# Optimization experiments

Hardware: AMD Instinct MI355X
Metric: run time of the kernel (lower is better)

The kernel has to match this reference:

```python
import jax, jax.numpy as jnp
import numpy as np

NUM_CLASSES = 19
IGNORE = 255
KLD_MARGIN = 3.0
DEC = 0.01
BOT_EPS, TOP_EPS = 1e-4, 1.0
# eight-corner neighbor offsets (size=1), order matches AAF layers.eightcorner_activation
EDGE_OFFS = ((-1, -1), (-1, 0), (-1, 1), (0, -1), (0, 1), (1, -1), (1, 0), (1, 1))


def _shift(x, dy, dx, pad_val):
    # Shift along H,W (axes 1,2): out[:, y, x] = x[:, y+dy, x+dx], padded with pad_val.
    pads = [(0, 0), (1, 1), (1, 1)] + [(0, 0)] * (x.ndim - 3)
    xp = jnp.pad(x, pads, constant_values=pad_val)
    h, w = x.shape[1], x.shape[2]
    return xp[:, 1 + dy:1 + dy + h, 1 + dx:1 + dx + w]


def _resize_bilinear_ac(x, oh, ow):
    # torch F.interpolate(mode='bilinear', align_corners=True) on NCHW.
    n, c, h, w = x.shape
    ys = jnp.linspace(0.0, h - 1.0, oh)
    xs = jnp.linspace(0.0, w - 1.0, ow)
    y0 = jnp.floor(ys).astype(jnp.int32); y1 = jnp.minimum(y0 + 1, h - 1)
    x0 = jnp.floor(xs).astype(jnp.int32); x1 = jnp.minimum(x0 + 1, w - 1)
    wy = (ys - y0).astype(x.dtype)[None, None, :, None]
    wx = (xs - x0).astype(x.dtype)[None, None, None, :]
    rows = x[:, :, y0, :] * (1.0 - wy) + x[:, :, y1, :] * wy  # (N,C,oh,W)
    return rows[:, :, :, x0] * (1.0 - wx) + rows[:, :, :, x1] * wx  # (N,C,oh,ow)


def setup_inputs() -> dict:
    key = jax.random.key(0)
    k1, k2 = jax.random.split(key)
    preds = jax.random.normal(k1, (2, NUM_CLASSES, 64, 64), dtype=jnp.float32)
    targets = jax.random.randint(k2, (2, 512, 512), 0, NUM_CLASSES, dtype=jnp.int32)
    w_edge = jnp.zeros((1, 1, 1, NUM_CLASSES, 1, 3), dtype=jnp.float32)
    w_not_edge = jnp.zeros((1, 1, 1, NUM_CLASSES, 1, 3), dtype=jnp.float32)
    return {"preds": preds, "targets": targets, "w_edge": w_edge, "w_not_edge": w_not_edge}


def reference(preds, targets, w_edge, w_not_edge):
    h, w = targets.shape[1], targets.shape[2]
    pred = _resize_bilinear_ac(preds, h, w)          # (N,C,H,W)
    prob = jax.nn.softmax(pred, axis=1)
    prob = jnp.transpose(prob, (0, 2, 3, 1))          # (N,H,W,C) NHWC layout used by AAF layers

    labels = targets                                  # (N,H,W)
    ign = labels == IGNORE
    one_label = jnp.where(ign, 0, labels)
    ohl = jax.nn.one_hot(one_label, NUM_CLASSES, dtype=jnp.float32)  # (N,H,W,C)
    ohl = jnp.where(ign[..., None], float(IGNORE), ohl)

    # edge/non-edge class weights: softmax over last dim, take index 0 -> (1,1,1,C,1)
    w_e = jax.nn.softmax(w_edge, axis=-1)[..., 0]
    w_ne = jax.nn.softmax(w_not_edge, axis=-1)[..., 0]

    # ignores_from_label: bidirectional ignore mask, neighbor order is reversed offsets
    ignore_c = labels > NUM_CLASSES - 1               # (N,H,W)
    ignore8 = jnp.stack([_shift(ignore_c, -dy, -dx, True) | ignore_c for dy, dx in EDGE_OFFS], axis=-1)
    not_ignore = ~ignore8[:, :, :, None, :]           # (N,H,W,1,8)

    # edges_from_label: neighbor label (padded with ignore_class) differs from center
    edge8 = jnp.stack([_shift(ohl, dy, dx, float(IGNORE)) != ohl for dy, dx in EDGE_OFFS], axis=-1)  # (N,H,W,C,8)
    edge = edge8 & not_ignore
    not_edge = (~edge) & not_ignore

    # eightcorner_activation on probabilities (zero padded)
    probs_paired = jnp.stack([_shift(prob, dy, dx, 0.0) for dy, dx in EDGE_OFFS], axis=-1)  # (N,H,W,C,8)
    p = prob[..., None]                               # (N,H,W,C,1)
    pc = jnp.clip(p, BOT_EPS, TOP_EPS)
    npc = jnp.clip(1.0 - p, BOT_EPS, TOP_EPS)
    ppc = jnp.clip(probs_paired, BOT_EPS, TOP_EPS)
    nppc = jnp.clip(1.0 - probs_paired, BOT_EPS, TOP_EPS)

    # binary KL divergence per class/neighbor
    kldiv = ppc * jnp.log(ppc / pc) + nppc * jnp.log(nppc / npc)  # (N,H,W,C,8)

    # per-pixel class weights: sum_c w[c]*one_hot[c] -> (N,H,W,1,1)
    we_map = jnp.sum(w_e * ohl[..., None], axis=3, keepdims=True)
    wne_map = jnp.sum(w_ne * ohl[..., None], axis=3, keepdims=True)

    edge_loss = jnp.maximum(0.0, KLD_MARGIN - kldiv) * we_map
    not_edge_loss = kldiv * wne_map

    # torch.mean over gathered nonzero indices == masked sum / count
    e_cnt = jnp.maximum(jnp.sum(edge), 1).astype(jnp.float32)
    ne_cnt = jnp.maximum(jnp.sum(not_edge), 1).astype(jnp.float32)
    e_mean = jnp.sum(jnp.where(edge, edge_loss, 0.0)) / e_cnt
    ne_mean = jnp.sum(jnp.where(not_edge, not_edge_loss, 0.0)) / ne_cnt

    return e_mean * 1.0 * DEC + ne_mean * 1.0 * DEC
```

## Files before the change

### kernel.cpp

```cpp
#include <hip/hip_runtime.h>
#include <stdint.h>


#define NC 19
#define HH 512
#define WW 512
#define NB 2
#define TS 16
#define HS 18
#define HP (HS * HS)
#define ATRS 20
#define PS 25
#define NBLK 2048
#define LOG2E 1.4426950408889634f
#define LN2 0.6931471805599453f
#define LOG2EPS -13.287712379549449f
#define K2F 4.3280851226668906f
#define K2PAD 4.328125f

typedef _Float16 f16x2 __attribute__((ext_vector_type(2)));

#if __has_builtin(__builtin_amdgcn_exp2f)
#define EXP2F(x) __builtin_amdgcn_exp2f(x)
#else
#define EXP2F(x) __expf((x) * LN2)
#endif

#if __has_builtin(__builtin_amdgcn_fdot2)
#define FDOT2(a, b, c) __builtin_amdgcn_fdot2((a), (b), (c), false)
#else
#define FDOT2(a, b, c) fmaf((float)(a)[1], (float)(b)[1], fmaf((float)(a)[0], (float)(b)[0], (c)))
#endif

struct Part { float es, ns; unsigned int cnt, pad; };

union U32F2 { uint32_t u; f16x2 h; };
__device__ __forceinline__ uint32_t bc_u32(f16x2 v) { U32F2 x; x.h = v; return x.u; }
__device__ __forceinline__ f16x2 bc_h2(uint32_t v) { U32F2 x; x.u = v; return x.h; }
__device__ __forceinline__ float extf(f16x2 v, int h) { return h ? (float)v[1] : (float)v[0]; }

union U16H { uint16_t u; _Float16 h; };
__device__ __forceinline__ uint32_t pack_TL(int lab, float T) {
    U16H t; t.h = (_Float16)T;
    return ((uint32_t)lab << 16) | (uint32_t)t.u;
}
__device__ __forceinline__ float TL_T(uint32_t tl) {
    U16H t; t.u = (uint16_t)(tl & 0xFFFFu);
    return (float)t.h;
}

template <bool KEEP>
__device__ __forceinline__ int pix_compute(const float* __restrict__ patch,
                                           const int* __restrict__ tg,
                                           int y, int x, int y0b, int x0b,
                                           uint32_t* __restrict__ ATrow,
                                           uint32_t* __restrict__ TLw,
                                           f16x2* __restrict__ Dh,
                                           float* __restrict__ SLp) {
    const bool oob = ((unsigned)y >= (unsigned)HH) | ((unsigned)x >= (unsigned)WW);
    if (oob) {
        const _Float16 aP = (_Float16)1e-4f;
        const uint32_t aPP = bc_u32((f16x2){aP, aP});
        const uint32_t aPL = bc_u32((f16x2){aP, (_Float16)0.0f});
        uint2 wv;
        wv.x = aPP; wv.y = aPP;
        *reinterpret_cast<uint2*>(ATrow + 0) = wv;
        *reinterpret_cast<uint2*>(ATrow + 2) = wv;
        *reinterpret_cast<uint2*>(ATrow + 4) = wv;
        *reinterpret_cast<uint2*>(ATrow + 6) = wv;
        wv.y = aPL;
        *reinterpret_cast<uint2*>(ATrow + 8) = wv;
        uint2 zv; zv.x = 0u; zv.y = 0u;
        *reinterpret_cast<uint2*>(ATrow + 10) = zv;
        *reinterpret_cast<uint2*>(ATrow + 12) = zv;
        *reinterpret_cast<uint2*>(ATrow + 14) = zv;
        *reinterpret_cast<uint2*>(ATrow + 16) = zv;
        *reinterpret_cast<uint2*>(ATrow + 18) = zv;
        *TLw = pack_TL(255, 0.0f);
        if (KEEP) {
            const _Float16 dP = (_Float16)LOG2EPS;
#pragma unroll
            for (int j = 0; j < 10; ++j)
                Dh[j] = (j < 9) ? (f16x2){dP, dP} : (f16x2){dP, (_Float16)0.0f};
            *SLp = 0.0f;
        }
        return 255;
    }

    const int lab = tg[(y << 9) + x];
    const float fy = (float)(y * 63) / 511.0f;
    const float fx = (float)(x * 63) / 511.0f;
    const int y0 = (int)fy, x0 = (int)fx;
    const float wy = fy - (float)y0, wx = fx - (float)x0;
    const int y1 = min(y0 + 1, 63), x1 = min(x0 + 1, 63);
    const float omwy = 1.0f - wy, omwx = 1.0f - wx;
    const float bw00 = omwy * omwx, bw01 = omwy * wx;
    const float bw10 = wy * omwx,   bw11 = wy * wx;
    const int o00 = (y0 - y0b) * 5 + (x0 - x0b);
    const int o01 = o00 + (x1 - x0);
    const int o10 = o00 + (y1 - y0) * 5;
    const int o11 = o10 + (x1 - x0);

    float v2[NC];
    float s = 0.0f;
#pragma unroll
    for (int c = 0; c < NC; ++c) {
        const float* pc_ = &patch[c * PS];
        const float vv = fmaf(pc_[o00], bw00, fmaf(pc_[o01], bw01,
                          fmaf(pc_[o10], bw10, pc_[o11] * bw11)));
        v2[c] = vv;
        s += EXP2F(vv);
    }
    const float lns2 = __log2f(s);

    float Tdd = 0.0f, SL = 0.0f;
#pragma unroll
    for (int jp = 0; jp < 10; jp += 2) {
        uint32_t aw0 = 0u, aw1 = 0u, lw0 = 0u, lw1 = 0u;
#pragma unroll
        for (int q = 0; q < 2; ++q) {
            const int j = jp + q;
            _Float16 a0h = (_Float16)0.0f, l0h = (_Float16)0.0f, d0h = (_Float16)0.0f;
            _Float16 a1h = (_Float16)0.0f, l1h = (_Float16)0.0f, d1h = (_Float16)0.0f;
            {
                const int c = 2 * j;
                const float lr = v2[c] - lns2;
                const float p = EXP2F(lr);
                const float la = fmaxf(lr, LOG2EPS);
                const float aa = fmaxf(p, 1e-4f);
                const float lb = __log2f(fmaxf(1.0f - p, 1e-4f));
                const float dd = la - lb;
                Tdd = fmaf(aa, dd, Tdd); SL += lb;
                a0h = (_Float16)aa; l0h = (_Float16)lb; d0h = (_Float16)dd;
            }
            if (2 * j + 1 < NC) {
                const int c = 2 * j + 1;
                const float lr = v2[c] - lns2;
                const float p = EXP2F(lr);
                const float la = fmaxf(lr, LOG2EPS);
                const float aa = fmaxf(p, 1e-4f);
                const float lb = __log2f(fmaxf(1.0f - p, 1e-4f));
                const float dd = la - lb;
                Tdd = fmaf(aa, dd, Tdd); SL += lb;
                a1h = (_Float16)aa; l1h = (_Float16)lb; d1h = (_Float16)dd;
            }
            if (q == 0) { aw0 = bc_u32((f16x2){a0h, a1h}); lw0 = bc_u32((f16x2){l0h, l1h}); }
            else        { aw1 = bc_u32((f16x2){a0h, a1h}); lw1 = bc_u32((f16x2){l0h, l1h}); }
            if (KEEP) Dh[j] = (f16x2){d0h, d1h};
        }
        uint2 av; av.x = aw0; av.y = aw1;
        uint2 lv; lv.x = lw0; lv.y = lw1;
        *reinterpret_cast<uint2*>(ATrow + jp) = av;
        *reinterpret_cast<uint2*>(ATrow + 10 + jp) = lv;
    }
    *TLw = pack_TL(lab, Tdd + SL);
    if (KEEP) *SLp = SL;
    return lab;
}

__global__ __launch_bounds__(256, 5) void k_fused(const float* __restrict__ preds,
                                                  const int* __restrict__ targets,
                                                  const float* __restrict__ w_edge,
                                                  const float* __restrict__ w_not_edge,
                                                  Part* __restrict__ pb) {
    __shared__ __align__(16) uint32_t AT[HP * ATRS];
    __shared__ uint32_t TL[HP];
    __shared__ float2 swen[NC];
    __shared__ float patch[NC * PS];
    __shared__ float r_es[4], r_ns[4];
    __shared__ unsigned int r_cnt[4];

    const int tid = threadIdx.x;
    const int bx = blockIdx.x, by = blockIdx.y, n = blockIdx.z;

    if (tid < NC) {
        float sw_e, sw_n;
        {
            float a = w_edge[tid * 3 + 0], b = w_edge[tid * 3 + 1], c = w_edge[tid * 3 + 2];
            float m = fmaxf(a, fmaxf(b, c));
            float ea = __expf(a - m), eb = __expf(b - m), ec = __expf(c - m);
            sw_e = (ea / (ea + eb + ec)) * LN2;
        }
        {
            float a = w_not_edge[tid * 3 + 0], b = w_not_edge[tid * 3 + 1], c = w_not_edge[tid * 3 + 2];
            float m = fmaxf(a, fmaxf(b, c));
            float ea = __expf(a - m), eb = __expf(b - m), ec = __expf(c - m);
            sw_n = (ea / (ea + eb + ec)) * LN2;
        }
        swen[tid] = make_float2(sw_e, sw_n);
    }

    const int* tg = targets + (n << 18);
    const float* pbase = preds + (size_t)n * NC * 4096;

    const int ty = tid >> 4, tx = tid & 15;
    const int hi = (ty + 1) * HS + (tx + 1);
    const int DOFF[8] = {-HS - 1, -HS, -HS + 1, -1, 1, HS - 1, HS, HS + 1};
    const int DY[8] = {-1, -1, -1, 0, 0, 1, 1, 1};
    const int DX[8] = {-1, 0, 1, -1, 1, -1, 0, 1};
    const f16x2 one2 = {(_Float16)1.0f, (_Float16)1.0f};
    const f16x2 k32 = {(_Float16)K2F, (_Float16)K2F};

    float e_s = 0.0f, ne_s = 0.0f;
    unsigned int cnt = 0;

    const int yT = max(by * TS - 1, 0), xL = max(bx * TS - 1, 0);
    const int y0b = (yT * 63) / 511, x0b = (xL * 63) / 511;
    for (int t = tid; t < NC * PS; t += 256) {
        const int c = t / PS, r = t - c * PS;
        const int ry = r / 5, rx = r - ry * 5;
        const int sy = min(y0b + ry, 63), sx = min(x0b + rx, 63);
        patch[t] = pbase[c * 4096 + (sy << 6) + sx] * LOG2E;
    }
    __syncthreads();

    if (tid < 68) {
        int i;
        if (tid < 18)      i = tid;
        else if (tid < 36) i = 306 + (tid - 18);
        else if (tid < 52) i = (tid - 35) * HS;
        else               i = (tid - 51) * HS + 17;
        const int hy = i / HS, hx = i - hy * HS;
        pix_compute<false>(patch, tg, by * TS + hy - 1, bx * TS + hx - 1,
                           y0b, x0b, &AT[i * ATRS], &TL[i], nullptr, nullptr);
    }

    const uint32_t* myrow = &AT[hi * ATRS];
    f16x2 Dh[10];
    float SL;
    const int lab = pix_compute<true>(patch, tg, by * TS + ty, bx * TS + tx,
                                      y0b, x0b, &AT[hi * ATRS], &TL[hi], Dh, &SL);
    const int plab = lab >> 1, hlab = lab & 1;
    const float aown = extf(bc_h2(myrow[plab]), hlab);
    const float llab = extf(bc_h2(myrow[10 + plab]), hlab);
    const float dlab = __log2f(aown) - llab;
    const float u = fmaf(aown, dlab, llab);
    __syncthreads();

    const bool interior_blk = (bx > 0) & (bx < 31) & (by > 0) & (by < 31);
    const bool deep_blk = (bx > 1) & (bx < 30) & (by > 1) & (by < 30);
    float es_o = 0.0f, ns_o = 0.0f;
    float es_w = 0.0f, ns_w = 0.0f;

    if (deep_blk) {
#pragma unroll
        for (int k = 0; k < 8; ++k) {
            const int np = hi + DOFF[k];
            const uint32_t tl = TL[np];
            const int nlab = (int)(tl >> 16);
            const float T_N = TL_T(tl);
            const uint32_t* rb = &AT[np * ATRS];
            const uint4 A0 = *reinterpret_cast<const uint4*>(rb);
            const uint4 A1 = *reinterpret_cast<const uint4*>(rb + 4);
            const uint2 A2 = *reinterpret_cast<const uint2*>(rb + 8);
            float acc = 0.0f;
            acc = FDOT2(bc_h2(A0.x), Dh[0], acc);
            acc = FDOT2(bc_h2(A0.y), Dh[1], acc);
            acc = FDOT2(bc_h2(A0.z), Dh[2], acc);
            acc = FDOT2(bc_h2(A0.w), Dh[3], acc);
            acc = FDOT2(bc_h2(A1.x), Dh[4], acc);
            acc = FDOT2(bc_h2(A1.y), Dh[5], acc);
            acc = FDOT2(bc_h2(A1.z), Dh[6], acc);
            acc = FDOT2(bc_h2(A1.w), Dh[7], acc);
            acc = FDOT2(bc_h2(A2.x), Dh[8], acc);
            acc = FDOT2(bc_h2(A2.y), Dh[9], acc);
            const float dot = T_N - acc - SL;
            const float aN = extf(bc_h2(rb[plab]), hlab);
            const float lN = extf(bc_h2(rb[10 + plab]), hlab);
            const float dN = __log2f(aN) - lN;
            const float klL = fmaf(aN, dN, lN) - fmaf(aN, dlab, llab);
            const float klR = u - fmaf(aown, dN, lN);
            const bool df = (lab != nlab);
            const float wg = df ? 1.0f : 0.0f;
            const float2 sw = swen[nlab];
            es_o = fmaf(wg, fmaxf(K2F - klL, 0.0f), es_o);
            ns_o += dot - wg * klL;
            es_w = fmaf(wg * sw.x, fmaxf(K2F - klR, 0.0f), es_w);
            ns_w = fmaf(-wg * sw.y, klR, ns_w);
            cnt += df ? ((2u << 16) | (NC - 2)) : NC;
        }
    } else if (interior_blk) {
        const int gy = by * TS + ty, gx = bx * TS + tx;
#pragma unroll
        for (int k = 0; k < 8; ++k) {
            const int np = hi + DOFF[k];
            const uint32_t tl = TL[np];
            const int nlab = (int)(tl >> 16);
            const float T_N = TL_T(tl);
            const uint32_t* rb = &AT[np * ATRS];
            const uint4 A0 = *reinterpret_cast<const uint4*>(rb);
            const uint4 A1 = *reinterpret_cast<const uint4*>(rb + 4);
            const uint2 A2 = *reinterpret_cast<const uint2*>(rb + 8);
            float acc = 0.0f;
            acc = FDOT2(bc_h2(A0.x), Dh[0], acc);
            acc = FDOT2(bc_h2(A0.y), Dh[1], acc);
            acc = FDOT2(bc_h2(A0.z), Dh[2], acc);
            acc = FDOT2(bc_h2(A0.w), Dh[3], acc);
            acc = FDOT2(bc_h2(A1.x), Dh[4], acc);
            acc = FDOT2(bc_h2(A1.y), Dh[5], acc);
            acc = FDOT2(bc_h2(A1.z), Dh[6], acc);
            acc = FDOT2(bc_h2(A1.w), Dh[7], acc);
            acc = FDOT2(bc_h2(A2.x), Dh[8], acc);
            acc = FDOT2(bc_h2(A2.y), Dh[9], acc);
            const float dot = T_N - acc - SL;
            const float aN = extf(bc_h2(rb[plab]), hlab);
            const float lN = extf(bc_h2(rb[10 + plab]), hlab);
            const float dN = __log2f(aN) - lN;
            const float klL = fmaf(aN, dN, lN) - fmaf(aN, dlab, llab);
            const bool df = (lab != nlab);
            const float wg = df ? 1.0f : 0.0f;
            const int gyN = gy + DY[k], gxN = gx + DX[k];
            const bool E = ((unsigned)(gyN - 16) < 480u) & ((unsigned)(gxN - 16) < 480u);
            if (E) {
                const float klR = u - fmaf(aown, dN, lN);
                const float2 sw = swen[nlab];
                es_o = fmaf(wg, fmaxf(K2F - klL, 0.0f), es_o);
                ns_o += dot - wg * klL;
                es_w = fmaf(wg * sw.x, fmaxf(K2F - klR, 0.0f), es_w);
                ns_w = fmaf(-wg * sw.y, klR, ns_w);
            } else {
                const int pn = nlab >> 1, hn = nlab & 1;
                const float aN2 = extf(bc_h2(rb[pn]), hn);
                const float lN2 = extf(bc_h2(rb[10 + pn]), hn);
                const float dN2 = __log2f(aN2) - lN2;
                const float ao = extf(bc_h2(myrow[pn]), hn);
                const float lo = extf(bc_h2(myrow[10 + pn]), hn);
                const float doo = __log2f(ao) - lo;
                const float klN = fmaf(aN2, dN2, lN2) - fmaf(aN2, doo, lo);
                es_o = fmaf(wg, fmaxf(K2F - klL, 0.0f) + fmaxf(K2F - klN, 0.0f), es_o);
                ns_o += dot - wg * (klL + klN);
            }
            cnt += df ? ((2u << 16) | (NC - 2)) : NC;
        }
    } else if (lab <= NC - 1) {
        const _Float16 aP = (_Float16)1e-4f, dP = (_Float16)LOG2EPS;
        const _Float16 tP = (_Float16)((float)aP * (float)dP);
#pragma unroll
        for (int k = 0; k < 8; ++k) {
            const int off = DOFF[k];
            const int rlab = (int)(TL[hi - off] >> 16);
            const bool rvalid = (rlab <= NC - 1);
            const int np = hi + off;
            const uint32_t tl = TL[np];
            const int nlab = (int)(tl >> 16);
            const bool isPad = (nlab == 255);
            float ek_k, nk_k;
            unsigned int pc;
            if (isPad) {
                float ekall = 0.0f;
#pragma unroll
                for (int j = 0; j < 10; j += 2) {
                    const uint2 lr = *reinterpret_cast<const uint2*>(myrow + 10 + j);
                    const f16x2 l20 = bc_h2(lr.x);
                    const f16x2 l21 = bc_h2(lr.y);
                    const f16x2 a20 = {aP, aP};
                    const f16x2 t20 = {tP, tP};
                    const f16x2 a21 = (j + 1 < 9) ? (f16x2){aP, aP} : (f16x2){aP, (_Float16)0.0f};
                    const f16x2 t21 = (j + 1 < 9) ? (f16x2){tP, tP} : (f16x2){tP, (_Float16)0.0f};
                    f16x2 kl0 = t20 - (a20 * Dh[j] + l20);
                    f16x2 kl1 = t21 - (a21 * Dh[j + 1] + l21);
                    f16x2 m0 = k32 - kl0, m1 = k32 - kl1;
                    m0[0] = m0[0] > (_Float16)0.0f ? m0[0] : (_Float16)0.0f;
                    m0[1] = m0[1] > (_Float16)0.0f ? m0[1] : (_Float16)0.0f;
                    m1[0] = m1[0] > (_Float16)0.0f ? m1[0] : (_Float16)0.0f;
                    m1[1] = m1[1] > (_Float16)0.0f ? m1[1] : (_Float16)0.0f;
                    ekall = FDOT2(m0, one2, ekall);
                    ekall = FDOT2(m1, one2, ekall);
                }
                ek_k = ekall - K2PAD;
                nk_k = 0.0f;
                pc = NC;
            } else {
                const float T_N = TL_T(tl);
                const uint32_t* rb = &AT[np * ATRS];
                const uint4 A0 = *reinterpret_cast<const uint4*>(rb);
                const uint4 A1 = *reinterpret_cast<const uint4*>(rb + 4);
                const uint2 A2 = *reinterpret_cast<const uint2*>(rb + 8);
                float acc = 0.0f;
                acc = FDOT2(bc_h2(A0.x), Dh[0], acc);
                acc = FDOT2(bc_h2(A0.y), Dh[1], acc);
                acc = FDOT2(bc_h2(A0.z), Dh[2], acc);
                acc = FDOT2(bc_h2(A0.w), Dh[3], acc);
                acc = FDOT2(bc_h2(A1.x), Dh[4], acc);
                acc = FDOT2(bc_h2(A1.y), Dh[5], acc);
                acc = FDOT2(bc_h2(A1.z), Dh[6], acc);
                acc = FDOT2(bc_h2(A1.w), Dh[7], acc);
                acc = FDOT2(bc_h2(A2.x), Dh[8], acc);
                acc = FDOT2(bc_h2(A2.y), Dh[9], acc);
                const float dot = T_N - acc - SL;
                const float aN = extf(bc_h2(rb[plab]), hlab);
                const float lN = extf(bc_h2(rb[10 + plab]), hlab);
                const float dN = __log2f(aN) - lN;
                const float klL = fmaf(aN, dN, lN) - fmaf(aN, dlab, llab);
                const int pn = nlab >> 1, hn = nlab & 1;
                const float aN2 = extf(bc_h2(rb[pn]), hn);
                const float lN2 = extf(bc_h2(rb[10 + pn]), hn);
                const float dN2 = __log2f(aN2) - lN2;
                const float ao = extf(bc_h2(myrow[pn]), hn);
                const float lo = extf(bc_h2(myrow[10 + pn]), hn);
                const float doo = __log2f(ao) - lo;
                const float klN = fmaf(aN2, dN2, lN2) - fmaf(aN2, doo, lo);
                const bool df = (lab != nlab);
                const float wg = df ? 1.0f : 0.0f;
                ek_k = wg * (fmaxf(K2F - klL, 0.0f) + fmaxf(K2F - klN, 0.0f));
                nk_k = dot - wg * (klL + klN);
                pc = df ? 2u : 0u;
            }
            const float vf = rvalid ? 1.0f : 0.0f;
            es_o = fmaf(vf, ek_k, es_o);
            ns_o = fmaf(vf, nk_k, ns_o);
            cnt += rvalid ? ((pc << 16) | (NC - pc)) : 0u;
        }
    }

    {
        const float2 swl = swen[lab <= NC - 1 ? lab : 0];
        e_s  = fmaf(es_o, swl.x, es_w);
        ne_s = fmaf(ns_o, swl.y, ns_w);
    }

#pragma unroll
    for (int off = 32; off > 0; off >>= 1) {
        e_s  += __shfl_down(e_s, off, 64);
        ne_s += __shfl_down(ne_s, off, 64);
        cnt  += __shfl_down(cnt, off, 64);
    }
    const int wid = tid >> 6, lane = tid & 63;
    if (lane == 0) { r_es[wid] = e_s; r_ns[wid] = ne_s; r_cnt[wid] = cnt; }
    __syncthreads();
    if (tid == 0) {
        float tes = 0.0f, tns = 0.0f;
        unsigned int tc = 0;
#pragma unroll
        for (int w = 0; w < 4; ++w) { tes += r_es[w]; tns += r_ns[w]; tc += r_cnt[w]; }
        const int bid = (blockIdx.z * gridDim.y + blockIdx.y) * gridDim.x + blockIdx.x;
        pb[bid].es = tes; pb[bid].ns = tns; pb[bid].cnt = tc; pb[bid].pad = 0;
    }
}

__global__ __launch_bounds__(256) void k_final(const Part* __restrict__ pb,
                                               float* __restrict__ out) {
    const int tid = threadIdx.x;
    double es = 0.0, ns = 0.0;
    long long ec = 0, nc = 0;
    for (int i = tid; i < NBLK; i += 256) {
        es += (double)pb[i].es; ns += (double)pb[i].ns;
        const unsigned int c = pb[i].cnt;
        ec += (long long)(c >> 16); nc += (long long)(c & 0xFFFFu);
    }
#pragma unroll
    for (int off = 32; off > 0; off >>= 1) {
        es += __shfl_down(es, off, 64);
        ns += __shfl_down(ns, off, 64);
        ec += __shfl_down(ec, off, 64);
        nc += __shfl_down(nc, off, 64);
    }
    __shared__ double ses[4], sns[4];
    __shared__ long long sec[4], snc[4];
    const int wid = tid >> 6, lane = tid & 63;
    if (lane == 0) { ses[wid] = es; sns[wid] = ns; sec[wid] = ec; snc[wid] = nc; }
    __syncthreads();
    if (tid == 0) {
        double tes = 0.0, tns = 0.0;
        long long tec = 0, tnc = 0;
#pragma unroll
        for (int w = 0; w < 4; ++w) { tes += ses[w]; tns += sns[w]; tec += sec[w]; tnc += snc[w]; }
        double ecd = (double)tec; if (ecd < 1.0) ecd = 1.0;
        double ncd = (double)tnc; if (ncd < 1.0) ncd = 1.0;
        out[0] = (float)((tes / ecd) * 0.01 + (tns / ncd) * 0.01);
    }
}

extern "C" void kernel_launch(void* const* d_in, const int* in_sizes, int n_in,
                              void* d_out, int out_size, void* d_ws, size_t ws_size,
                              hipStream_t stream) {
    const float* preds      = (const float*)d_in[0];
    const int*   targets    = (const int*)d_in[1];
    const float* w_edge     = (const float*)d_in[2];
    const float* w_not_edge = (const float*)d_in[3];

    Part* pb = (Part*)d_ws;

    dim3 grid(WW / TS, HH / TS, NB);
    k_fused<<<grid, 256, 0, stream>>>(preds, targets, w_edge, w_not_edge, pb);
    k_final<<<1, 256, 0, stream>>>(pb, (float*)d_out);
}
```

Before: 97.20 us.

## Use 32x16 tiles with 512 threads and store log-ratio instead of log(1-p)

Tiles grow from 16x16 to 32x16 pixels with 512 threads per block. This lowers the share of halo pixels recomputed per block and halves the number of block partials. The per-pixel softmax now reuses the exp values with a reciprocal instead of a second exp2. The shared row stores d=la-lb in place of lb, and pad halo rows are no longer written and are handled analytically. This adds extra log2 calls in the neighbour and pad paths, and the larger blocks may change occupancy.

```diff
diff --git a/kernel.cpp b/kernel.cpp
--- a/kernel.cpp
+++ b/kernel.cpp
@@ -6,17 +6,21 @@
 #define HH 512
 #define WW 512
 #define NB 2
-#define TS 16
+#define TSY 32
+#define TSX 16
 #define HS 18
-#define HP (HS * HS)
+#define VS 34
+#define HP (VS * HS)
 #define ATRS 20
-#define PS 25
-#define NBLK 2048
+#define PS 35
+#define NBLK 1024
 #define LOG2E 1.4426950408889634f
 #define LN2 0.6931471805599453f
 #define LOG2EPS -13.287712379549449f
 #define K2F 4.3280851226668906f
-#define K2PAD 4.328125f
+#define A_PAD 1e-4f
+#define T1_PAD (-0.0013287712379549449f)
+#define T_PAD (-0.025246653521143952f)
 
 typedef _Float16 f16x2 __attribute__((ext_vector_type(2)));
 
@@ -32,12 +36,11 @@
 #define FDOT2(a, b, c) fmaf((float)(a)[1], (float)(b)[1], fmaf((float)(a)[0], (float)(b)[0], (c)))
 #endif
 
-struct Part { float es, ns; unsigned int cnt, pad; };
+struct Part { float es, ns; unsigned int ec, nc; };
 
 union U32F2 { uint32_t u; f16x2 h; };
 __device__ __forceinline__ uint32_t bc_u32(f16x2 v) { U32F2 x; x.h = v; return x.u; }
 __device__ __forceinline__ f16x2 bc_h2(uint32_t v) { U32F2 x; x.u = v; return x.h; }
-__device__ __forceinline__ float extf(f16x2 v, int h) { return h ? (float)v[1] : (float)v[0]; }
 
 union U16H { uint16_t u; _Float16 h; };
 __device__ __forceinline__ uint32_t pack_TL(int lab, float T) {
@@ -59,24 +62,7 @@
                                            float* __restrict__ SLp) {
     const bool oob = ((unsigned)y >= (unsigned)HH) | ((unsigned)x >= (unsigned)WW);
     if (oob) {
-        const _Float16 aP = (_Float16)1e-4f;
-        const uint32_t aPP = bc_u32((f16x2){aP, aP});
-        const uint32_t aPL = bc_u32((f16x2){aP, (_Float16)0.0f});
-        uint2 wv;
-        wv.x = aPP; wv.y = aPP;
-        *reinterpret_cast<uint2*>(ATrow + 0) = wv;
-        *reinterpret_cast<uint2*>(ATrow + 2) = wv;
-        *reinterpret_cast<uint2*>(ATrow + 4) = wv;
-        *reinterpret_cast<uint2*>(ATrow + 6) = wv;
-        wv.y = aPL;
-        *reinterpret_cast<uint2*>(ATrow + 8) = wv;
-        uint2 zv; zv.x = 0u; zv.y = 0u;
-        *reinterpret_cast<uint2*>(ATrow + 10) = zv;
-        *reinterpret_cast<uint2*>(ATrow + 12) = zv;
-        *reinterpret_cast<uint2*>(ATrow + 14) = zv;
-        *reinterpret_cast<uint2*>(ATrow + 16) = zv;
-        *reinterpret_cast<uint2*>(ATrow + 18) = zv;
-        *TLw = pack_TL(255, 0.0f);
+        *TLw = pack_TL(255, T_PAD);
         if (KEEP) {
             const _Float16 dP = (_Float16)LOG2EPS;
 #pragma unroll
@@ -94,71 +80,73 @@
     const float wy = fy - (float)y0, wx = fx - (float)x0;
     const int y1 = min(y0 + 1, 63), x1 = min(x0 + 1, 63);
     const float omwy = 1.0f - wy, omwx = 1.0f - wx;
-    const float bw00 = omwy * omwx, bw01 = omwy * wx;
-    const float bw10 = wy * omwx,   bw11 = wy * wx;
+    const float w00 = omwy * omwx, w01 = omwy * wx;
+    const float w10 = wy * omwx,   w11 = wy * wx;
     const int o00 = (y0 - y0b) * 5 + (x0 - x0b);
     const int o01 = o00 + (x1 - x0);
     const int o10 = o00 + (y1 - y0) * 5;
     const int o11 = o10 + (x1 - x0);
 
-    float v2[NC];
+    float v2[NC], w[NC];
     float s = 0.0f;
 #pragma unroll
     for (int c = 0; c < NC; ++c) {
         const float* pc_ = &patch[c * PS];
-        const float vv = fmaf(pc_[o00], bw00, fmaf(pc_[o01], bw01,
-                          fmaf(pc_[o10], bw10, pc_[o11] * bw11)));
+        const float vv = fmaf(pc_[o00], w00, fmaf(pc_[o01], w01,
+                          fmaf(pc_[o10], w10, pc_[o11] * w11)));
         v2[c] = vv;
-        s += EXP2F(vv);
-    }
+        const float e = EXP2F(vv);
+        w[c] = e;
+        s += e;
+    }
+    const float inv = 1.0f / s;
     const float lns2 = __log2f(s);
 
     float Tdd = 0.0f, SL = 0.0f;
 #pragma unroll
     for (int jp = 0; jp < 10; jp += 2) {
-        uint32_t aw0 = 0u, aw1 = 0u, lw0 = 0u, lw1 = 0u;
+        uint32_t aw0 = 0u, aw1 = 0u, dw0 = 0u, dw1 = 0u;
 #pragma unroll
         for (int q = 0; q < 2; ++q) {
             const int j = jp + q;
-            _Float16 a0h = (_Float16)0.0f, l0h = (_Float16)0.0f, d0h = (_Float16)0.0f;
-            _Float16 a1h = (_Float16)0.0f, l1h = (_Float16)0.0f, d1h = (_Float16)0.0f;
+            _Float16 a0h, d0h, a1h = (_Float16)0.0f, d1h = (_Float16)0.0f;
             {
                 const int c = 2 * j;
-                const float lr = v2[c] - lns2;
-                const float p = EXP2F(lr);
-                const float la = fmaxf(lr, LOG2EPS);
+                const float p = w[c] * inv;
+                const float la = fmaxf(v2[c] - lns2, LOG2EPS);
                 const float aa = fmaxf(p, 1e-4f);
                 const float lb = __log2f(fmaxf(1.0f - p, 1e-4f));
-                const float dd = la - lb;
-                Tdd = fmaf(aa, dd, Tdd); SL += lb;
-                a0h = (_Float16)aa; l0h = (_Float16)lb; d0h = (_Float16)dd;
+                a0h = (_Float16)aa;
+                d0h = (_Float16)(la - lb);
+                Tdd = fmaf((float)a0h, (float)d0h, Tdd);
+                SL += lb;
             }
             if (2 * j + 1 < NC) {
                 const int c = 2 * j + 1;
-                const float lr = v2[c] - lns2;
-                const float p = EXP2F(lr);
-                const float la = fmaxf(lr, LOG2EPS);
+                const float p = w[c] * inv;
+                const float la = fmaxf(v2[c] - lns2, LOG2EPS);
                 const float aa = fmaxf(p, 1e-4f);
                 const float lb = __log2f(fmaxf(1.0f - p, 1e-4f));
-                const float dd = la - lb;
-                Tdd = fmaf(aa, dd, Tdd); SL += lb;
-                a1h = (_Float16)aa; l1h = (_Float16)lb; d1h = (_Float16)dd;
+                a1h = (_Float16)aa;
+                d1h = (_Float16)(la - lb);
+                Tdd = fmaf((float)a1h, (float)d1h, Tdd);
+                SL += lb;
             }
-            if (q == 0) { aw0 = bc_u32((f16x2){a0h, a1h}); lw0 = bc_u32((f16x2){l0h, l1h}); }
-            else        { aw1 = bc_u32((f16x2){a0h, a1h}); lw1 = bc_u32((f16x2){l0h, l1h}); }
+            if (q == 0) { aw0 = bc_u32((f16x2){a0h, a1h}); dw0 = bc_u32((f16x2){d0h, d1h}); }
+            else        { aw1 = bc_u32((f16x2){a0h, a1h}); dw1 = bc_u32((f16x2){d0h, d1h}); }
             if (KEEP) Dh[j] = (f16x2){d0h, d1h};
         }
         uint2 av; av.x = aw0; av.y = aw1;
-        uint2 lv; lv.x = lw0; lv.y = lw1;
+        uint2 dv; dv.x = dw0; dv.y = dw1;
         *reinterpret_cast<uint2*>(ATrow + jp) = av;
-        *reinterpret_cast<uint2*>(ATrow + 10 + jp) = lv;
+        *reinterpret_cast<uint2*>(ATrow + 10 + jp) = dv;
     }
     *TLw = pack_TL(lab, Tdd + SL);
     if (KEEP) *SLp = SL;
     return lab;
 }
 
-__global__ __launch_bounds__(256, 5) void k_fused(const float* __restrict__ preds,
+__global__ __launch_bounds__(512, 6) void k_fused(const float* __restrict__ preds,
                                                   const int* __restrict__ targets,
                                                   const float* __restrict__ w_edge,
                                                   const float* __restrict__ w_not_edge,
@@ -167,9 +155,6 @@
     __shared__ uint32_t TL[HP];
     __shared__ float2 swen[NC];
     __shared__ float patch[NC * PS];
-    __shared__ float r_es[4], r_ns[4];
-    __shared__ unsigned int r_cnt[4];
-
     const int tid = threadIdx.x;
     const int bx = blockIdx.x, by = blockIdx.y, n = blockIdx.z;
 
@@ -198,15 +183,13 @@
     const int DOFF[8] = {-HS - 1, -HS, -HS + 1, -1, 1, HS - 1, HS, HS + 1};
     const int DY[8] = {-1, -1, -1, 0, 0, 1, 1, 1};
     const int DX[8] = {-1, 0, 1, -1, 1, -1, 0, 1};
-    const f16x2 one2 = {(_Float16)1.0f, (_Float16)1.0f};
-    const f16x2 k32 = {(_Float16)K2F, (_Float16)K2F};
 
     float e_s = 0.0f, ne_s = 0.0f;
     unsigned int cnt = 0;
 
-    const int yT = max(by * TS - 1, 0), xL = max(bx * TS - 1, 0);
+    const int yT = max(by * TSY - 1, 0), xL = max(bx * TSX - 1, 0);
     const int y0b = (yT * 63) / 511, x0b = (xL * 63) / 511;
-    for (int t = tid; t < NC * PS; t += 256) {
+    for (int t = tid; t < NC * PS; t += 512) {
         const int c = t / PS, r = t - c * PS;
         const int ry = r / 5, rx = r - ry * 5;
         const int sy = min(y0b + ry, 63), sx = min(x0b + rx, 63);
@@ -214,31 +197,31 @@
     }
     __syncthreads();
 
-    if (tid < 68) {
+    if (tid < 100) {
         int i;
         if (tid < 18)      i = tid;
-        else if (tid < 36) i = 306 + (tid - 18);
-        else if (tid < 52) i = (tid - 35) * HS;
-        else               i = (tid - 51) * HS + 17;
+        else if (tid < 36) i = 33 * HS + (tid - 18);
+        else if (tid < 68) i = (tid - 35) * HS;
+        else               i = (tid - 67) * HS + 17;
         const int hy = i / HS, hx = i - hy * HS;
-        pix_compute<false>(patch, tg, by * TS + hy - 1, bx * TS + hx - 1,
+        pix_compute<false>(patch, tg, by * TSY + hy - 1, bx * TSX + hx - 1,
                            y0b, x0b, &AT[i * ATRS], &TL[i], nullptr, nullptr);
     }
 
-    const uint32_t* myrow = &AT[hi * ATRS];
     f16x2 Dh[10];
     float SL;
-    const int lab = pix_compute<true>(patch, tg, by * TS + ty, bx * TS + tx,
+    const int lab = pix_compute<true>(patch, tg, by * TSY + ty, bx * TSX + tx,
                                       y0b, x0b, &AT[hi * ATRS], &TL[hi], Dh, &SL);
-    const int plab = lab >> 1, hlab = lab & 1;
-    const float aown = extf(bc_h2(myrow[plab]), hlab);
-    const float llab = extf(bc_h2(myrow[10 + plab]), hlab);
-    const float dlab = __log2f(aown) - llab;
+    const uint32_t* myrow = &AT[hi * ATRS];
+    const _Float16* hM = reinterpret_cast<const _Float16*>(myrow);
+    const float aown = (float)hM[lab];
+    const float dlab = (float)hM[20 + lab];
+    const float llab = __log2f(aown) - dlab;
     const float u = fmaf(aown, dlab, llab);
     __syncthreads();
 
-    const bool interior_blk = (bx > 0) & (bx < 31) & (by > 0) & (by < 31);
-    const bool deep_blk = (bx > 1) & (bx < 30) & (by > 1) & (by < 30);
+    const bool interior_blk = (bx > 0) & (bx < 31) & (by > 0) & (by < 15);
+    const bool deep_blk = (bx > 1) & (bx < 30) & (by > 1) & (by < 14);
     float es_o = 0.0f, ns_o = 0.0f;
     float es_w = 0.0f, ns_w = 0.0f;
 
@@ -250,6 +233,7 @@
             const int nlab = (int)(tl >> 16);
             const float T_N = TL_T(tl);
             const uint32_t* rb = &AT[np * ATRS];
+            const _Float16* hN = reinterpret_cast<const _Float16*>(rb);
             const uint4 A0 = *reinterpret_cast<const uint4*>(rb);
             const uint4 A1 = *reinterpret_cast<const uint4*>(rb + 4);
             const uint2 A2 = *reinterpret_cast<const uint2*>(rb + 8);
@@ -265,10 +249,10 @@
             acc = FDOT2(bc_h2(A2.x), Dh[8], acc);
             acc = FDOT2(bc_h2(A2.y), Dh[9], acc);
             const float dot = T_N - acc - SL;
-            const float aN = extf(bc_h2(rb[plab]), hlab);
-            const float lN = extf(bc_h2(rb[10 + plab]), hlab);
-            const float dN = __log2f(aN) - lN;
-            const float klL = fmaf(aN, dN, lN) - fmaf(aN, dlab, llab);
+            const float aN = (float)hN[lab];
+            const float dN = (float)hN[20 + lab];
+            const float lN = __log2f(aN) - dN;
+            const float klL = fmaf(aN, dN - dlab, lN - llab);
             const float klR = u - fmaf(aown, dN, lN);
             const bool df = (lab != nlab);
             const float wg = df ? 1.0f : 0.0f;
@@ -280,7 +264,7 @@
             cnt += df ? ((2u << 16) | (NC - 2)) : NC;
         }
     } else if (interior_blk) {
-        const int gy = by * TS + ty, gx = bx * TS + tx;
+        const int gy = by * TSY + ty, gx = bx * TSX + tx;
 #pragma unroll
         for (int k = 0; k < 8; ++k) {
             const int np = hi + DOFF[k];
@@ -288,6 +272,7 @@
             const int nlab = (int)(tl >> 16);
             const float T_N = TL_T(tl);
             const uint32_t* rb = &AT[np * ATRS];
+            const _Float16* hN = reinterpret_cast<const _Float16*>(rb);
             const uint4 A0 = *reinterpret_cast<const uint4*>(rb);
             const uint4 A1 = *reinterpret_cast<const uint4*>(rb + 4);
             const uint2 A2 = *reinterpret_cast<const uint2*>(rb + 8);
@@ -303,14 +288,15 @@
             acc = FDOT2(bc_h2(A2.x), Dh[8], acc);
             acc = FDOT2(bc_h2(A2.y), Dh[9], acc);
             const float dot = T_N - acc - SL;
-            const float aN = extf(bc_h2(rb[plab]), hlab);
-            const float lN = extf(bc_h2(rb[10 + plab]), hlab);
-            const float dN = __log2f(aN) - lN;
-            const float klL = fmaf(aN, dN, lN) - fmaf(aN, dlab, llab);
+            const float aN = (float)hN[lab];
+            const float dN = (float)hN[20 + lab];
+            const float lN = __log2f(aN) - dN;
+            const float klL = fmaf(aN, dN - dlab, lN - llab);
             const bool df = (lab != nlab);
             const float wg = df ? 1.0f : 0.0f;
             const int gyN = gy + DY[k], gxN = gx + DX[k];
-            const bool E = ((unsigned)(gyN - 16) < 480u) & ((unsigned)(gxN - 16) < 480u);
+            const bool E = ((unsigned)(gyN - TSY) < (HH - 2 * TSY)) &
+                           ((unsigned)(gxN - TSX) < (WW - 2 * TSX));
             if (E) {
                 const float klR = u - fmaf(aown, dN, lN);
                 const float2 sw = swen[nlab];
@@ -319,22 +305,19 @@
                 es_w = fmaf(wg * sw.x, fmaxf(K2F - klR, 0.0f), es_w);
                 ns_w = fmaf(-wg * sw.y, klR, ns_w);
             } else {
-                const int pn = nlab >> 1, hn = nlab & 1;
-                const float aN2 = extf(bc_h2(rb[pn]), hn);
-                const float lN2 = extf(bc_h2(rb[10 + pn]), hn);
-                const float dN2 = __log2f(aN2) - lN2;
-                const float ao = extf(bc_h2(myrow[pn]), hn);
-                const float lo = extf(bc_h2(myrow[10 + pn]), hn);
-                const float doo = __log2f(ao) - lo;
-                const float klN = fmaf(aN2, dN2, lN2) - fmaf(aN2, doo, lo);
+                const float aN2 = (float)hN[nlab];
+                const float dN2 = (float)hN[20 + nlab];
+                const float lN2 = __log2f(aN2) - dN2;
+                const float aOo = (float)hM[nlab];
+                const float dOo = (float)hM[20 + nlab];
+                const float lOo = __log2f(aOo) - dOo;
+                const float klN = fmaf(aN2, dN2 - dOo, lN2 - lOo);
                 es_o = fmaf(wg, fmaxf(K2F - klL, 0.0f) + fmaxf(K2F - klN, 0.0f), es_o);
                 ns_o += dot - wg * (klL + klN);
             }
             cnt += df ? ((2u << 16) | (NC - 2)) : NC;
         }
     } else if (lab <= NC - 1) {
-        const _Float16 aP = (_Float16)1e-4f, dP = (_Float16)LOG2EPS;
-        const _Float16 tP = (_Float16)((float)aP * (float)dP);
 #pragma unroll
         for (int k = 0; k < 8; ++k) {
             const int off = DOFF[k];
@@ -349,30 +332,26 @@
             if (isPad) {
                 float ekall = 0.0f;
 #pragma unroll
-                for (int j = 0; j < 10; j += 2) {
-                    const uint2 lr = *reinterpret_cast<const uint2*>(myrow + 10 + j);
-                    const f16x2 l20 = bc_h2(lr.x);
-                    const f16x2 l21 = bc_h2(lr.y);
-                    const f16x2 a20 = {aP, aP};
-                    const f16x2 t20 = {tP, tP};
-                    const f16x2 a21 = (j + 1 < 9) ? (f16x2){aP, aP} : (f16x2){aP, (_Float16)0.0f};
-                    const f16x2 t21 = (j + 1 < 9) ? (f16x2){tP, tP} : (f16x2){tP, (_Float16)0.0f};
-                    f16x2 kl0 = t20 - (a20 * Dh[j] + l20);
-                    f16x2 kl1 = t21 - (a21 * Dh[j + 1] + l21);
-                    f16x2 m0 = k32 - kl0, m1 = k32 - kl1;
-                    m0[0] = m0[0] > (_Float16)0.0f ? m0[0] : (_Float16)0.0f;
-                    m0[1] = m0[1] > (_Float16)0.0f ? m0[1] : (_Float16)0.0f;
-                    m1[0] = m1[0] > (_Float16)0.0f ? m1[0] : (_Float16)0.0f;
-                    m1[1] = m1[1] > (_Float16)0.0f ? m1[1] : (_Float16)0.0f;
-                    ekall = FDOT2(m0, one2, ekall);
-                    ekall = FDOT2(m1, one2, ekall);
+                for (int j = 0; j < 10; ++j) {
+                    const f16x2 ap = bc_h2(myrow[j]);
+                    const float a0 = (float)ap[0], d0 = (float)Dh[j][0];
+                    const float l0 = __log2f(a0) - d0;
+                    const float kl0 = T1_PAD - fmaf(A_PAD, d0, l0);
+                    ekall += fmaxf(K2F - kl0, 0.0f);
+                    if (2 * j + 1 < NC) {
+                        const float a1 = (float)ap[1], d1 = (float)Dh[j][1];
+                        const float l1 = __log2f(a1) - d1;
+                        const float kl1 = T1_PAD - fmaf(A_PAD, d1, l1);
+                        ekall += fmaxf(K2F - kl1, 0.0f);
+                    }
                 }
-                ek_k = ekall - K2PAD;
+                ek_k = ekall;
                 nk_k = 0.0f;
                 pc = NC;
             } else {
                 const float T_N = TL_T(tl);
                 const uint32_t* rb = &AT[np * ATRS];
+                const _Float16* hN = reinterpret_cast<const _Float16*>(rb);
                 const uint4 A0 = *reinterpret_cast<const uint4*>(rb);
                 const uint4 A1 = *reinterpret_cast<const uint4*>(rb + 4);
                 const uint2 A2 = *reinterpret_cast<const uint2*>(rb + 8);
@@ -388,18 +367,17 @@
                 acc = FDOT2(bc_h2(A2.x), Dh[8], acc);
                 acc = FDOT2(bc_h2(A2.y), Dh[9], acc);
                 const float dot = T_N - acc - SL;
-                const float aN = extf(bc_h2(rb[plab]), hlab);
-                const float lN = extf(bc_h2(rb[10 + plab]), hlab);
-                const float dN = __log2f(aN) - lN;
-                const float klL = fmaf(aN, dN, lN) - fmaf(aN, dlab, llab);
-                const int pn = nlab >> 1, hn = nlab & 1;
-                const float aN2 = extf(bc_h2(rb[pn]), hn);
-                const float lN2 = extf(bc_h2(rb[10 + pn]), hn);
-                const float dN2 = __log2f(aN2) - lN2;
-                const float ao = extf(bc_h2(myrow[pn]), hn);
-                const float lo = extf(bc_h2(myrow[10 + pn]), hn);
-                const float doo = __log2f(ao) - lo;
-                const float klN = fmaf(aN2, dN2, lN2) - fmaf(aN2, doo, lo);
+                const float aN = (float)hN[lab];
+                const float dN = (float)hN[20 + lab];
+                const float lN = __log2f(aN) - dN;
+                const float klL = fmaf(aN, dN - dlab, lN - llab);
+                const float aN2 = (float)hN[nlab];
+                const float dN2 = (float)hN[20 + nlab];
+                const float lN2 = __log2f(aN2) - dN2;
+                const float aOo = (float)hM[nlab];
+                const float dOo = (float)hM[20 + nlab];
+                const float lOo = __log2f(aOo) - dOo;
+                const float klN = fmaf(aN2, dN2 - dOo, lN2 - lOo);
                 const bool df = (lab != nlab);
                 const float wg = df ? 1.0f : 0.0f;
                 ek_k = wg * (fmaxf(K2F - klL, 0.0f) + fmaxf(K2F - klN, 0.0f));
@@ -425,16 +403,22 @@
         ne_s += __shfl_down(ne_s, off, 64);
         cnt  += __shfl_down(cnt, off, 64);
     }
+    float* r_es = patch;
+    float* r_ns = patch + 8;
+    unsigned int* r_cnt = reinterpret_cast<unsigned int*>(patch + 16);
     const int wid = tid >> 6, lane = tid & 63;
     if (lane == 0) { r_es[wid] = e_s; r_ns[wid] = ne_s; r_cnt[wid] = cnt; }
     __syncthreads();
     if (tid == 0) {
         float tes = 0.0f, tns = 0.0f;
-        unsigned int tc = 0;
-#pragma unroll
-        for (int w = 0; w < 4; ++w) { tes += r_es[w]; tns += r_ns[w]; tc += r_cnt[w]; }
+        unsigned int tec = 0, tnc = 0;
+#pragma unroll
+        for (int w = 0; w < 8; ++w) {
+            tes += r_es[w]; tns += r_ns[w];
+            tec += r_cnt[w] >> 16; tnc += r_cnt[w] & 0xFFFFu;
+        }
         const int bid = (blockIdx.z * gridDim.y + blockIdx.y) * gridDim.x + blockIdx.x;
-        pb[bid].es = tes; pb[bid].ns = tns; pb[bid].cnt = tc; pb[bid].pad = 0;
+        pb[bid].es = tes; pb[bid].ns = tns; pb[bid].ec = tec; pb[bid].nc = tnc;
     }
 }
 
@@ -445,8 +429,7 @@
     long long ec = 0, nc = 0;
     for (int i = tid; i < NBLK; i += 256) {
         es += (double)pb[i].es; ns += (double)pb[i].ns;
-        const unsigned int c = pb[i].cnt;
-        ec += (long long)(c >> 16); nc += (long long)(c & 0xFFFFu);
+        ec += (long long)pb[i].ec; nc += (long long)pb[i].nc;
     }
 #pragma unroll
     for (int off = 32; off > 0; off >>= 1) {
@@ -481,7 +464,7 @@
 
     Part* pb = (Part*)d_ws;
 
-    dim3 grid(WW / TS, HH / TS, NB);
-    k_fused<<<grid, 256, 0, stream>>>(preds, targets, w_edge, w_not_edge, pb);
+    dim3 grid(WW / TSX, HH / TSY, NB);
+    k_fused<<<grid, 512, 0, stream>>>(preds, targets, w_edge, w_not_edge, pb);
     k_final<<<1, 256, 0, stream>>>(pb, (float*)d_out);
 }
```

After: 113.8 us. +17.1%, slower.
